# Kernel tuning notes

Measured on AMD Instinct MI355X. Metric: run time of the kernel, lower is better.

Reference implementation:

```python
import jax, jax.numpy as jnp
import numpy as np

D_MODEL = 1024
N_HEADS = 32
HEAD_DIM = D_MODEL // N_HEADS
EPS = 1e-5


def setup_inputs() -> dict:
    key = jax.random.key(0)
    ks = jax.random.split(key, 6)
    B, S = 2, 2048
    scale = 1.0 / np.sqrt(D_MODEL)
    return {
        "x": jax.random.normal(ks[0], (B, S, D_MODEL), dtype=jnp.float32),
        "Wqkv_w": jax.random.normal(ks[1], (3 * D_MODEL, D_MODEL), dtype=jnp.float32) * scale,
        "Wqkv_b": jax.random.normal(ks[2], (3 * D_MODEL,), dtype=jnp.float32) * 0.01,
        "gn_w": jnp.ones((D_MODEL,), dtype=jnp.float32),
        "gn_b": jnp.zeros((D_MODEL,), dtype=jnp.float32),
        "out_w": jax.random.normal(ks[3], (D_MODEL, D_MODEL), dtype=jnp.float32) * scale,
        "out_b": jax.random.normal(ks[4], (D_MODEL,), dtype=jnp.float32) * 0.01,
    }


def reference(x, Wqkv_w, Wqkv_b, gn_w, gn_b, out_w, out_b):
    B, S, Dm = x.shape
    H, Dh = N_HEADS, HEAD_DIM
    # QKV projection
    qkv = x @ Wqkv_w.T + Wqkv_b                      # [B,S,3*Dm]
    qkv = qkv.reshape(B, S, 3, H, Dh)
    q, k, v = qkv[:, :, 0], qkv[:, :, 1], qkv[:, :, 2]  # each [B,S,H,Dh]
    # Linear (softmax-free) attention; dropout p=0 -> identity
    a = jnp.einsum('bthd,bshd->bhts', q, k)          # [B,H,S,S]
    ctx = jnp.einsum('bhts,bshd->bthd', a, v)        # [B,S,H,Dh]
    # GroupNorm(num_groups=H, num_channels=Dm) on transposed (B, Dm, S):
    # normalizes jointly over (Dh channels, S positions) per (batch, group)
    g = ctx.transpose(0, 2, 3, 1)                    # [B,H,Dh,S]
    mean = g.mean(axis=(2, 3), keepdims=True)
    var = ((g - mean) ** 2).mean(axis=(2, 3), keepdims=True)
    gh = (g - mean) * jax.lax.rsqrt(var + EPS)
    gh = gh * gn_w.reshape(H, Dh, 1) + gn_b.reshape(H, Dh, 1)
    ctx = gh.transpose(0, 3, 1, 2).reshape(B, S, Dm)  # back to [B,S,Dm]
    return ctx @ out_w.T + out_b
```

## Files before the change

kernel.cpp:

```cpp
#include <hip/hip_runtime.h>
#include <hip/hip_bf16.h>
#include <stdint.h>

typedef unsigned short ushort_t;
typedef __attribute__((ext_vector_type(4))) float f32x4;
typedef __attribute__((ext_vector_type(8))) short short8;

#define SS 2048
#define ROWS 4096
#define EPS 1e-5f

__device__ __forceinline__ unsigned short f2bf(float f) {
  unsigned int u = __float_as_uint(f);
  u += 0x7FFF + ((u >> 16) & 1);
  return (unsigned short)(u >> 16);
}
__device__ __forceinline__ float bf2f(short s) {
  return __uint_as_float(((unsigned int)(unsigned short)s) << 16);
}

#define GLDS16(g, l)                                                        \
  __builtin_amdgcn_global_load_lds((__attribute__((address_space(1))) void*)(g), \
                                   (__attribute__((address_space(3))) void*)(l), 16, 0, 0)

__global__ __launch_bounds__(256) void f2b2_kernel(const float* __restrict__ a,
                                                   ushort_t* __restrict__ oa, int n4a,
                                                   const float* __restrict__ b,
                                                   ushort_t* __restrict__ ob, int n4b) {
  const int stride = gridDim.x * blockDim.x;
  const int total = n4a + n4b;
  for (int i = blockIdx.x * blockDim.x + threadIdx.x; i < total; i += stride) {
    const float4 v = (i < n4a) ? reinterpret_cast<const float4*>(a)[i]
                               : reinterpret_cast<const float4*>(b)[i - n4a];
    ushort4 o;
    o.x = f2bf(v.x); o.y = f2bf(v.y); o.z = f2bf(v.z); o.w = f2bf(v.w);
    if (i < n4a) reinterpret_cast<ushort4*>(oa)[i] = o;
    else         reinterpret_cast<ushort4*>(ob)[i - n4a] = o;
  }
}

#define MF(d, va, vb) d = __builtin_amdgcn_mfma_f32_16x16x32_bf16(va, vb, d, 0, 0, 0)
#define LD8(p) (*reinterpret_cast<const short8*>(p))

__global__ __launch_bounds__(512, 2) void gemm1_pipe(const ushort_t* __restrict__ A,
                                                     const ushort_t* __restrict__ B,
                                                     const float* __restrict__ bias,
                                                     ushort_t* __restrict__ C) {
  __shared__ __align__(16) ushort_t lds[4 * 14336];
  const int tid = threadIdx.x;
  const int wid = tid >> 6, lane = tid & 63;
  const int bm = blockIdx.x * 256, bn = blockIdx.y * 192;
  const int wm = wid >> 2, wn = wid & 3;

  const int srow = lane >> 2;
  const int scol = ((lane & 3) ^ ((lane >> 3) & 3)) * 8;
  const int widb = (wid < 6) ? wid : 0;
  const ushort_t* gA0 = A + (size_t)(bm + wid * 16 + srow) * 1024 + scol;
  const ushort_t* gA1 = A + (size_t)(bm + (8 + wid) * 16 + srow) * 1024 + scol;
  const ushort_t* gB0 = B + (size_t)(bn + widb * 16 + srow) * 1024 + scol;
  const ushort_t* gB1 = B + (size_t)(bn + (6 + widb) * 16 + srow) * 1024 + scol;

  const int lf = lane & 15, kf = lane >> 4;
  const int flip = ((lane >> 1) & 3) << 4;
  const int aBase = (((wm * 128 + lf) * 64 + kf * 16) ^ flip) >> 1;
  const int bBase = ((((wn * 48 + lf) * 64 + kf * 16) ^ flip) >> 1) + 8192;

  f32x4 acc[8][3] = {};

#define STAGE_A(t)                                                           \
  { ushort_t* d = lds + (((t) & 3) * 14336);                                 \
    GLDS16(gA0 + (t) * 32, d + wid * 512);                                   \
    GLDS16(gA1 + (t) * 32, d + (8 + wid) * 512); }
#define STAGE_B(t)                                                           \
  if (wid < 6) { ushort_t* d = lds + (((t) & 3) * 14336) + 8192;             \
    GLDS16(gB0 + (t) * 32, d + wid * 512);                                   \
    GLDS16(gB1 + (t) * 32, d + (6 + wid) * 512); }

  STAGE_A(0) STAGE_B(0)
  STAGE_A(1) STAGE_B(1)
  STAGE_A(2) STAGE_B(2)
  if (wid < 6) { asm volatile("s_waitcnt vmcnt(8)" ::: "memory"); }
  else         { asm volatile("s_waitcnt vmcnt(4)" ::: "memory"); }
  __builtin_amdgcn_s_barrier();
  __builtin_amdgcn_sched_barrier(0);

#define K_TILE(t, DO_STAGE, VM6, VM2)                                        \
  { const ushort_t* Lb = lds + (((t) & 3) * 14336);                          \
    short8 bv0 = LD8(Lb + bBase);                                            \
    short8 bv1 = LD8(Lb + bBase + 512);                                      \
    short8 bv2 = LD8(Lb + bBase + 1024);                                     \
    short8 a0 = LD8(Lb + aBase);                                             \
    short8 a1 = LD8(Lb + aBase + 512);                                       \
    short8 a2 = LD8(Lb + aBase + 1024);                                      \
    short8 a3 = LD8(Lb + aBase + 1536);                                      \
    if (DO_STAGE) STAGE_A((t) + 3)                                           \
    __builtin_amdgcn_s_setprio(1);                                           \
    MF(acc[0][0], a0, bv0); MF(acc[1][0], a1, bv0);                          \
    MF(acc[0][1], a0, bv1); MF(acc[1][1], a1, bv1);                          \
    MF(acc[0][2], a0, bv2); MF(acc[1][2], a1, bv2);                          \
    MF(acc[2][0], a2, bv0); MF(acc[3][0], a3, bv0);                          \
    MF(acc[2][1], a2, bv1); MF(acc[3][1], a3, bv1);                          \
    MF(acc[2][2], a2, bv2); MF(acc[3][2], a3, bv2);                          \
    __builtin_amdgcn_s_setprio(0);                                           \
    a0 = LD8(Lb + aBase + 2048);                                             \
    a1 = LD8(Lb + aBase + 2560);                                             \
    a2 = LD8(Lb + aBase + 3072);                                             \
    a3 = LD8(Lb + aBase + 3584);                                             \
    if (DO_STAGE) STAGE_B((t) + 3)                                           \
    __builtin_amdgcn_s_setprio(1);                                           \
    MF(acc[4][0], a0, bv0); MF(acc[5][0], a1, bv0);                          \
    MF(acc[4][1], a0, bv1); MF(acc[5][1], a1, bv1);                          \
    MF(acc[4][2], a0, bv2); MF(acc[5][2], a1, bv2);                          \
    MF(acc[6][0], a2, bv0); MF(acc[7][0], a3, bv0);                          \
    MF(acc[6][1], a2, bv1); MF(acc[7][1], a3, bv1);                          \
    MF(acc[6][2], a2, bv2); MF(acc[7][2], a3, bv2);                          \
    __builtin_amdgcn_s_setprio(0);                                           \
    __builtin_amdgcn_sched_barrier(0);                                       \
    if (wid < 6) { asm volatile("s_waitcnt vmcnt(" #VM6 ")" ::: "memory"); } \
    else         { asm volatile("s_waitcnt vmcnt(" #VM2 ")" ::: "memory"); } \
    __builtin_amdgcn_s_barrier();                                            \
    __builtin_amdgcn_sched_barrier(0); }

#pragma unroll 1
  for (int t = 0; t < 29; ++t) K_TILE(t, 1, 8, 4)
  K_TILE(29, 0, 4, 2)
  K_TILE(30, 0, 0, 0)
  K_TILE(31, 0, 0, 0)

  const int crow = bm + wm * 128 + (lane >> 4) * 4;
  const int ccol = bn + wn * 48 + (lane & 15);
#pragma unroll
  for (int m = 0; m < 8; ++m)
#pragma unroll
    for (int n = 0; n < 3; ++n) {
      const int col = ccol + n * 16;
      const float bb = bias[col];
#pragma unroll
      for (int j = 0; j < 4; ++j)
        C[(size_t)(crow + m * 16 + j) * 3072 + col] = f2bf(acc[m][n][j] + bb);
    }
#undef K_TILE
#undef STAGE_A
#undef STAGE_B
}

__global__ __launch_bounds__(256, 2) void gemm2_pipe(const ushort_t* __restrict__ A,
                                                     const ushort_t* __restrict__ B,
                                                     const float* __restrict__ bias,
                                                     float* __restrict__ C) {
  __shared__ __align__(16) ushort_t lds[4 * 6144];
  const int tid = threadIdx.x;
  const int wid = tid >> 6, lane = tid & 63;
  const int bm = blockIdx.x * 64, bn = blockIdx.y * 128;
  if (bm >= 2048) { B += (size_t)1024 * 1024; bias += 1024; }
  const int wm = wid >> 1, wn = wid & 1;

  const int srow = lane >> 2;
  const int scol = ((lane & 3) ^ ((lane >> 3) & 3)) * 8;
  const ushort_t* gA  = A + (size_t)(bm + wid * 16 + srow) * 1024 + scol;
  const ushort_t* gB0 = B + (size_t)(bn + wid * 16 + srow) * 1024 + scol;
  const ushort_t* gB1 = B + (size_t)(bn + (4 + wid) * 16 + srow) * 1024 + scol;

  const int lf = lane & 15, kf = lane >> 4;
  const int flip = ((lane >> 1) & 3) << 4;
  const int aBase = (((wm * 32 + lf) * 64 + kf * 16) ^ flip) >> 1;
  const int bBase = ((((wn * 64 + lf) * 64 + kf * 16) ^ flip) >> 1) + 2048;

  f32x4 acc[2][4] = {};

#define STAGE2(t)                                                            \
  { ushort_t* d = lds + (((t) & 3) * 6144);                                  \
    GLDS16(gA + (t) * 32, d + wid * 512);                                    \
    GLDS16(gB0 + (t) * 32, d + 2048 + wid * 512);                            \
    GLDS16(gB1 + (t) * 32, d + 2048 + (4 + wid) * 512); }

  STAGE2(0) STAGE2(1) STAGE2(2)
  asm volatile("s_waitcnt vmcnt(6)" ::: "memory");
  __builtin_amdgcn_s_barrier();
  __builtin_amdgcn_sched_barrier(0);

#define K_TILE2(t, DO_STAGE, VM)                                             \
  { const ushort_t* Lb = lds + (((t) & 3) * 6144);                           \
    short8 bv0 = LD8(Lb + bBase);                                            \
    short8 bv1 = LD8(Lb + bBase + 512);                                      \
    short8 bv2 = LD8(Lb + bBase + 1024);                                     \
    short8 bv3 = LD8(Lb + bBase + 1536);                                     \
    short8 a0 = LD8(Lb + aBase);                                             \
    short8 a1 = LD8(Lb + aBase + 512);                                       \
    if (DO_STAGE) STAGE2((t) + 3)                                            \
    __builtin_amdgcn_s_setprio(1);                                           \
    MF(acc[0][0], a0, bv0); MF(acc[1][0], a1, bv0);                          \
    MF(acc[0][1], a0, bv1); MF(acc[1][1], a1, bv1);                          \
    MF(acc[0][2], a0, bv2); MF(acc[1][2], a1, bv2);                          \
    MF(acc[0][3], a0, bv3); MF(acc[1][3], a1, bv3);                          \
    __builtin_amdgcn_s_setprio(0);                                           \
    __builtin_amdgcn_sched_barrier(0);                                       \
    asm volatile("s_waitcnt vmcnt(" #VM ")" ::: "memory");                   \
    __builtin_amdgcn_s_barrier();                                            \
    __builtin_amdgcn_sched_barrier(0); }

#pragma unroll 1
  for (int t = 0; t < 29; ++t) K_TILE2(t, 1, 6)
  K_TILE2(29, 0, 3)
  K_TILE2(30, 0, 0)
  K_TILE2(31, 0, 0)

  const int crow = bm + wm * 32 + (lane >> 4) * 4;
  const int ccol = bn + wn * 64 + lf;
#pragma unroll
  for (int m = 0; m < 2; ++m)
#pragma unroll
    for (int n = 0; n < 4; ++n) {
      const int col = ccol + n * 16;
      const float bb = bias[col];
#pragma unroll
      for (int j = 0; j < 4; ++j)
        C[(size_t)(crow + m * 16 + j) * 1024 + col] = acc[m][n][j] + bb;
    }
#undef K_TILE2
#undef STAGE2
}

__global__ __launch_bounds__(256) void kv_partial(const ushort_t* __restrict__ qkvb,
                                                  float* __restrict__ KVp) {
  __shared__ float kt[64 * 32];
  __shared__ float vt[64 * 32];
  const int blk = blockIdx.x;
  const int bh = blk >> 5;
  const int ch = blk & 31;
  const int b = bh >> 5, h = bh & 31;
  const int tid = threadIdx.x;
  const int r = tid >> 2, cg = (tid & 3) * 8;
  const ushort_t* kp = qkvb + (size_t)(b * SS + ch * 64 + r) * 3072 + 1024 + h * 32 + cg;
  const short8 k8 = *(const short8*)kp;
  const short8 v8 = *(const short8*)(kp + 1024);
#pragma unroll
  for (int i = 0; i < 8; ++i) {
    kt[r * 32 + cg + i] = bf2f(k8[i]);
    vt[r * 32 + cg + i] = bf2f(v8[i]);
  }
  __syncthreads();
  const int d = tid & 31, eg = tid >> 5;
  float acc[4] = {0.f, 0.f, 0.f, 0.f};
#pragma unroll 8
  for (int ss = 0; ss < 64; ++ss) {
    const float vv = vt[ss * 32 + d];
#pragma unroll
    for (int i = 0; i < 4; ++i)
      acc[i] += kt[ss * 32 + eg * 4 + i] * vv;
  }
  float* o = KVp + ((size_t)bh * 32 + ch) * 1024 + (eg * 4) * 32 + d;
#pragma unroll
  for (int i = 0; i < 4; ++i) o[i * 32] = acc[i];
}

__global__ __launch_bounds__(256) void kv_reduce(const float* __restrict__ KVp,
                                                 float* __restrict__ KV) {
  const int bh = blockIdx.x;
  const int tid = threadIdx.x;
  const float* base = KVp + (size_t)bh * 32768 + tid * 4;
  float4 s = make_float4(0.f, 0.f, 0.f, 0.f);
  for (int c = 0; c < 32; ++c) {
    const float4 v = *(const float4*)(base + c * 1024);
    s.x += v.x; s.y += v.y; s.z += v.z; s.w += v.w;
  }
  *(float4*)&KV[(size_t)bh * 1024 + tid * 4] = s;
}

__global__ __launch_bounds__(256) void ctx_kernel(const ushort_t* __restrict__ qkvb,
                                                  const float* __restrict__ KV,
                                                  ushort_t* __restrict__ ctxb,
                                                  float2* __restrict__ partials) {
  __shared__ float kvs[1024];
  __shared__ float red[8];
  const int blk = blockIdx.x;
  const int bh = blk >> 3, tt = blk & 7;
  const int b = bh >> 5, h = bh & 31;
  const int tid = threadIdx.x;
  for (int i = tid; i < 1024; i += 256) kvs[i] = KV[(size_t)bh * 1024 + i];
  __syncthreads();
  const int t = tt * 256 + tid;
  const ushort_t* qrow = qkvb + ((size_t)(b * SS + t)) * 3072 + h * 32;
  float q[32];
#pragma unroll
  for (int g = 0; g < 4; ++g) {
    const short8 qv = *(const short8*)(qrow + g * 8);
#pragma unroll
    for (int i = 0; i < 8; ++i) q[g * 8 + i] = bf2f(qv[i]);
  }
  float o[32];
#pragma unroll
  for (int d = 0; d < 32; ++d) o[d] = 0.f;
#pragma unroll
  for (int e = 0; e < 32; ++e) {
    const float qe = q[e];
    const float* kr = &kvs[e * 32];
#pragma unroll
    for (int d = 0; d < 32; ++d) o[d] += qe * kr[d];
  }
  float sum = 0.f, sq = 0.f;
#pragma unroll
  for (int d = 0; d < 32; ++d) { sum += o[d]; sq += o[d] * o[d]; }
  ushort_t* crow = ctxb + ((size_t)(b * SS + t)) * 1024 + h * 32;
#pragma unroll
  for (int g = 0; g < 4; ++g) {
    short8 ov;
#pragma unroll
    for (int i = 0; i < 8; ++i) ov[i] = (short)f2bf(o[g * 8 + i]);
    *(short8*)(crow + g * 8) = ov;
  }
#pragma unroll
  for (int off = 32; off > 0; off >>= 1) {
    sum += __shfl_down(sum, off);
    sq  += __shfl_down(sq, off);
  }
  const int wave = tid >> 6, lane = tid & 63;
  if (lane == 0) { red[wave * 2] = sum; red[wave * 2 + 1] = sq; }
  __syncthreads();
  if (tid == 0) {
    const float s = red[0] + red[2] + red[4] + red[6];
    const float q2 = red[1] + red[3] + red[5] + red[7];
    partials[blk] = make_float2(s, q2);
  }
}

__global__ __launch_bounds__(256) void fold_kernel(const float* __restrict__ W2,
                                                   const float* __restrict__ b2,
                                                   const float* __restrict__ gw,
                                                   const float* __restrict__ gb,
                                                   const float2* __restrict__ partials,
                                                   ushort_t* __restrict__ W2s,
                                                   float* __restrict__ bias2) {
  __shared__ float sS[1024], sT[1024];
  __shared__ float sMean[32], sRstd[32];
  const int b = blockIdx.y;
  const int tid = threadIdx.x;
  if (tid < 32) {
    float s = 0.f, q = 0.f;
    for (int i = 0; i < 8; ++i) {
      const float2 p = partials[(b * 32 + tid) * 8 + i];
      s += p.x; q += p.y;
    }
    const float mean = s * (1.f / 65536.f);
    const float var = q * (1.f / 65536.f) - mean * mean;
    sMean[tid] = mean; sRstd[tid] = rsqrtf(var + EPS);
  }
  __syncthreads();
  {
    const int c0 = tid * 4;
    const float mean = sMean[c0 >> 5], rstd = sRstd[c0 >> 5];
    const float4 w = *(const float4*)&gw[c0];
    const float4 g = *(const float4*)&gb[c0];
    sS[c0]     = rstd * w.x;  sT[c0]     = g.x - mean * rstd * w.x;
    sS[c0 + 1] = rstd * w.y;  sT[c0 + 1] = g.y - mean * rstd * w.y;
    sS[c0 + 2] = rstd * w.z;  sT[c0 + 2] = g.z - mean * rstd * w.z;
    sS[c0 + 3] = rstd * w.w;  sT[c0 + 3] = g.w - mean * rstd * w.w;
  }
  __syncthreads();
  const int row = blockIdx.x * 16 + (tid >> 4);
  const int l16 = tid & 15;
  float part = 0.f;
  for (int k = 0; k < 16; ++k) {
    const int c = k * 64 + l16 * 4;
    const float4 w2v = *(const float4*)&W2[(size_t)row * 1024 + c];
    ushort4 o;
    o.x = f2bf(w2v.x * sS[c]);
    o.y = f2bf(w2v.y * sS[c + 1]);
    o.z = f2bf(w2v.z * sS[c + 2]);
    o.w = f2bf(w2v.w * sS[c + 3]);
    *(ushort4*)&W2s[(size_t)b * 1048576 + (size_t)row * 1024 + c] = o;
    part += w2v.x * sT[c] + w2v.y * sT[c + 1] + w2v.z * sT[c + 2] + w2v.w * sT[c + 3];
  }
#pragma unroll
  for (int off = 8; off > 0; off >>= 1) part += __shfl_down(part, off, 16);
  if (l16 == 0) bias2[b * 1024 + row] = b2[row] + part;
}

extern "C" void kernel_launch(void* const* d_in, const int* in_sizes, int n_in,
                              void* d_out, int out_size, void* d_ws, size_t ws_size,
                              hipStream_t stream) {
  const float* x  = (const float*)d_in[0];
  const float* w1 = (const float*)d_in[1];
  const float* b1 = (const float*)d_in[2];
  const float* gw = (const float*)d_in[3];
  const float* gb = (const float*)d_in[4];
  const float* w2 = (const float*)d_in[5];
  const float* b2 = (const float*)d_in[6];
  float* out = (float*)d_out;

  char* ws = (char*)d_ws;
  ushort_t* Xb    = (ushort_t*)(ws);
  float*    KVp   = (float*)(ws);
  ushort_t* W1b   = (ushort_t*)(ws + 8388608);
  ushort_t* qkvb  = (ushort_t*)(ws + 16777216);
  ushort_t* ctxb  = (ushort_t*)(ws + 41943040);
  ushort_t* W2s   = (ushort_t*)(ws + 50331648);
  float*    bias2 = (float*)(ws + 54525952);
  float*    KV    = (float*)(ws + 54534144);
  float2*   partials = (float2*)(ws + 54796288);

  f2b2_kernel<<<2048, 256, 0, stream>>>(x, Xb, ROWS * 1024 / 4, w1, W1b, 3072 * 1024 / 4);
  gemm1_pipe<<<dim3(16, 16), 512, 0, stream>>>(Xb, W1b, b1, qkvb);
  kv_partial<<<2048, 256, 0, stream>>>(qkvb, KVp);
  kv_reduce<<<64, 256, 0, stream>>>(KVp, KV);
  ctx_kernel<<<512, 256, 0, stream>>>(qkvb, KV, ctxb, partials);
  fold_kernel<<<dim3(64, 2), 256, 0, stream>>>(w2, b2, gw, gb, partials, W2s, bias2);
  gemm2_pipe<<<dim3(64, 8), 256, 0, stream>>>(ctxb, W2s, bias2, out);
}
```

Before: 88.92 us.

## Compute GroupNorm stats analytically from Q covariance and KV, drop fold kernel

GroupNorm mean and variance are now derived in closed form from per-head Q^T Q covariance, Q column sums and the KV matrix, which the partial kernel accumulates alongside KV. Normalization is applied directly when ctx is written, so the fold kernel that rescaled W2 per batch is removed. The separate kv_reduce launch is merged into the ctx kernel, and W2 is cast to bf16 in the existing conversion kernel. This cuts launches and the W2 fold pass, but each ctx block redundantly reduces 32 partials of two matrices, and computing variance as E[x^2] minus mean^2 in fp32 may lose precision.

```diff
diff --git a/kernel.cpp b/kernel.cpp
--- a/kernel.cpp
+++ b/kernel.cpp
@@ -23,19 +23,23 @@
   __builtin_amdgcn_global_load_lds((__attribute__((address_space(1))) void*)(g), \
                                    (__attribute__((address_space(3))) void*)(l), 16, 0, 0)
 
-__global__ __launch_bounds__(256) void f2b2_kernel(const float* __restrict__ a,
+__global__ __launch_bounds__(256) void f2b3_kernel(const float* __restrict__ a,
                                                    ushort_t* __restrict__ oa, int n4a,
                                                    const float* __restrict__ b,
-                                                   ushort_t* __restrict__ ob, int n4b) {
+                                                   ushort_t* __restrict__ ob, int n4b,
+                                                   const float* __restrict__ c,
+                                                   ushort_t* __restrict__ oc, int n4c) {
   const int stride = gridDim.x * blockDim.x;
-  const int total = n4a + n4b;
+  const int total = n4a + n4b + n4c;
   for (int i = blockIdx.x * blockDim.x + threadIdx.x; i < total; i += stride) {
-    const float4 v = (i < n4a) ? reinterpret_cast<const float4*>(a)[i]
-                               : reinterpret_cast<const float4*>(b)[i - n4a];
+    const float* src; ushort_t* dst; int idx;
+    if (i < n4a)            { src = a; dst = oa; idx = i; }
+    else if (i < n4a + n4b) { src = b; dst = ob; idx = i - n4a; }
+    else                    { src = c; dst = oc; idx = i - n4a - n4b; }
+    const float4 v = reinterpret_cast<const float4*>(src)[idx];
     ushort4 o;
     o.x = f2bf(v.x); o.y = f2bf(v.y); o.z = f2bf(v.z); o.w = f2bf(v.w);
-    if (i < n4a) reinterpret_cast<ushort4*>(oa)[i] = o;
-    else         reinterpret_cast<ushort4*>(ob)[i - n4a] = o;
+    reinterpret_cast<ushort4*>(dst)[idx] = o;
   }
 }
 
@@ -152,7 +156,6 @@
   const int tid = threadIdx.x;
   const int wid = tid >> 6, lane = tid & 63;
   const int bm = blockIdx.x * 64, bn = blockIdx.y * 128;
-  if (bm >= 2048) { B += (size_t)1024 * 1024; bias += 1024; }
   const int wm = wid >> 1, wn = wid & 1;
 
   const int srow = lane >> 2;
@@ -221,8 +224,11 @@
 #undef STAGE2
 }
 
-__global__ __launch_bounds__(256) void kv_partial(const ushort_t* __restrict__ qkvb,
-                                                  float* __restrict__ KVp) {
+__global__ __launch_bounds__(256) void kvq_partial(const ushort_t* __restrict__ qkvb,
+                                                   float* __restrict__ KVp,
+                                                   float* __restrict__ Qcovp,
+                                                   float* __restrict__ qsump) {
+  __shared__ float qt[64 * 32];
   __shared__ float kt[64 * 32];
   __shared__ float vt[64 * 32];
   const int blk = blockIdx.x;
@@ -231,60 +237,119 @@
   const int b = bh >> 5, h = bh & 31;
   const int tid = threadIdx.x;
   const int r = tid >> 2, cg = (tid & 3) * 8;
-  const ushort_t* kp = qkvb + (size_t)(b * SS + ch * 64 + r) * 3072 + 1024 + h * 32 + cg;
-  const short8 k8 = *(const short8*)kp;
-  const short8 v8 = *(const short8*)(kp + 1024);
+  const ushort_t* base = qkvb + (size_t)(b * SS + ch * 64 + r) * 3072 + h * 32 + cg;
+  const short8 q8 = LD8(base);
+  const short8 k8 = LD8(base + 1024);
+  const short8 v8 = LD8(base + 2048);
 #pragma unroll
   for (int i = 0; i < 8; ++i) {
+    qt[r * 32 + cg + i] = bf2f(q8[i]);
     kt[r * 32 + cg + i] = bf2f(k8[i]);
     vt[r * 32 + cg + i] = bf2f(v8[i]);
   }
   __syncthreads();
   const int d = tid & 31, eg = tid >> 5;
-  float acc[4] = {0.f, 0.f, 0.f, 0.f};
-#pragma unroll 8
+  float kv[4] = {0.f, 0.f, 0.f, 0.f};
+  float qc[4] = {0.f, 0.f, 0.f, 0.f};
+#pragma unroll 4
   for (int ss = 0; ss < 64; ++ss) {
     const float vv = vt[ss * 32 + d];
-#pragma unroll
-    for (int i = 0; i < 4; ++i)
-      acc[i] += kt[ss * 32 + eg * 4 + i] * vv;
-  }
-  float* o = KVp + ((size_t)bh * 32 + ch) * 1024 + (eg * 4) * 32 + d;
-#pragma unroll
-  for (int i = 0; i < 4; ++i) o[i * 32] = acc[i];
-}
-
-__global__ __launch_bounds__(256) void kv_reduce(const float* __restrict__ KVp,
-                                                 float* __restrict__ KV) {
-  const int bh = blockIdx.x;
-  const int tid = threadIdx.x;
-  const float* base = KVp + (size_t)bh * 32768 + tid * 4;
-  float4 s = make_float4(0.f, 0.f, 0.f, 0.f);
-  for (int c = 0; c < 32; ++c) {
-    const float4 v = *(const float4*)(base + c * 1024);
-    s.x += v.x; s.y += v.y; s.z += v.z; s.w += v.w;
-  }
-  *(float4*)&KV[(size_t)bh * 1024 + tid * 4] = s;
-}
-
-__global__ __launch_bounds__(256) void ctx_kernel(const ushort_t* __restrict__ qkvb,
-                                                  const float* __restrict__ KV,
-                                                  ushort_t* __restrict__ ctxb,
-                                                  float2* __restrict__ partials) {
-  __shared__ float kvs[1024];
-  __shared__ float red[8];
+    const float qd = qt[ss * 32 + d];
+#pragma unroll
+    for (int i = 0; i < 4; ++i) {
+      kv[i] += kt[ss * 32 + eg * 4 + i] * vv;
+      qc[i] += qt[ss * 32 + eg * 4 + i] * qd;
+    }
+  }
+  float* okv = KVp + ((size_t)bh * 32 + ch) * 1024 + (eg * 4) * 32 + d;
+  float* oqc = Qcovp + ((size_t)bh * 32 + ch) * 1024 + (eg * 4) * 32 + d;
+#pragma unroll
+  for (int i = 0; i < 4; ++i) { okv[i * 32] = kv[i]; oqc[i * 32] = qc[i]; }
+  if (tid < 32) {
+    float s = 0.f;
+    for (int ss = 0; ss < 64; ++ss) s += qt[ss * 32 + tid];
+    qsump[((size_t)bh * 32 + ch) * 32 + tid] = s;
+  }
+}
+
+__global__ __launch_bounds__(256) void ctx_norm_kernel(const ushort_t* __restrict__ qkvb,
+                                                       const float* __restrict__ KVp,
+                                                       const float* __restrict__ Qcovp,
+                                                       const float* __restrict__ qsump,
+                                                       const float* __restrict__ gw,
+                                                       const float* __restrict__ gb,
+                                                       ushort_t* __restrict__ ghb) {
+  __shared__ float kvs[1024], qcov[1024];
+  __shared__ float qsums[32], gws[32], gbs[32];
+  __shared__ float red[16];
+  __shared__ float sstats[2];
   const int blk = blockIdx.x;
   const int bh = blk >> 3, tt = blk & 7;
   const int b = bh >> 5, h = bh & 31;
   const int tid = threadIdx.x;
-  for (int i = tid; i < 1024; i += 256) kvs[i] = KV[(size_t)bh * 1024 + i];
+  {
+    const float* kbase = KVp + (size_t)bh * 32768 + tid * 4;
+    const float* qbase = Qcovp + (size_t)bh * 32768 + tid * 4;
+    float4 sk = make_float4(0.f, 0.f, 0.f, 0.f);
+    float4 sq = make_float4(0.f, 0.f, 0.f, 0.f);
+    for (int c = 0; c < 32; ++c) {
+      const float4 k4 = *(const float4*)(kbase + c * 1024);
+      const float4 q4 = *(const float4*)(qbase + c * 1024);
+      sk.x += k4.x; sk.y += k4.y; sk.z += k4.z; sk.w += k4.w;
+      sq.x += q4.x; sq.y += q4.y; sq.z += q4.z; sq.w += q4.w;
+    }
+    *(float4*)&kvs[tid * 4] = sk;
+    *(float4*)&qcov[tid * 4] = sq;
+  }
+  if (tid < 32) {
+    float s = 0.f;
+    for (int c = 0; c < 32; ++c) s += qsump[((size_t)bh * 32 + c) * 32 + tid];
+    qsums[tid] = s;
+    gws[tid] = gw[h * 32 + tid];
+    gbs[tid] = gb[h * 32 + tid];
+  }
   __syncthreads();
+  {
+    const int d = tid & 31, ig = tid >> 5;
+    float e2p = 0.f;
+#pragma unroll
+    for (int ii = 0; ii < 4; ++ii) {
+      const int i = ig * 4 + ii;
+      float t = 0.f;
+#pragma unroll
+      for (int j = 0; j < 32; ++j) t += qcov[i * 32 + j] * kvs[j * 32 + d];
+      e2p += kvs[i * 32 + d] * t;
+    }
+#pragma unroll
+    for (int off = 32; off > 0; off >>= 1) e2p += __shfl_down(e2p, off);
+    float mp = 0.f;
+    if (tid < 32) {
+      float rs = 0.f;
+      for (int dd = 0; dd < 32; ++dd) rs += kvs[tid * 32 + ((dd + tid) & 31)];
+      mp = rs * qsums[tid];
+    }
+#pragma unroll
+    for (int off = 32; off > 0; off >>= 1) mp += __shfl_down(mp, off);
+    const int wave = tid >> 6, lane = tid & 63;
+    if (lane == 0) { red[wave] = e2p; red[8 + wave] = mp; }
+    __syncthreads();
+    if (tid == 0) {
+      const float E2 = red[0] + red[1] + red[2] + red[3];
+      const float MS = red[8] + red[9] + red[10] + red[11];
+      const float mean = MS * (1.f / 65536.f);
+      const float var = E2 * (1.f / 65536.f) - mean * mean;
+      sstats[0] = mean;
+      sstats[1] = rsqrtf(var + EPS);
+    }
+    __syncthreads();
+  }
+  const float mean = sstats[0], rstd = sstats[1];
   const int t = tt * 256 + tid;
   const ushort_t* qrow = qkvb + ((size_t)(b * SS + t)) * 3072 + h * 32;
   float q[32];
 #pragma unroll
   for (int g = 0; g < 4; ++g) {
-    const short8 qv = *(const short8*)(qrow + g * 8);
+    const short8 qv = LD8(qrow + g * 8);
 #pragma unroll
     for (int i = 0; i < 8; ++i) q[g * 8 + i] = bf2f(qv[i]);
   }
@@ -298,82 +363,17 @@
 #pragma unroll
     for (int d = 0; d < 32; ++d) o[d] += qe * kr[d];
   }
-  float sum = 0.f, sq = 0.f;
-#pragma unroll
-  for (int d = 0; d < 32; ++d) { sum += o[d]; sq += o[d] * o[d]; }
-  ushort_t* crow = ctxb + ((size_t)(b * SS + t)) * 1024 + h * 32;
+  ushort_t* crow = ghb + ((size_t)(b * SS + t)) * 1024 + h * 32;
 #pragma unroll
   for (int g = 0; g < 4; ++g) {
     short8 ov;
 #pragma unroll
-    for (int i = 0; i < 8; ++i) ov[i] = (short)f2bf(o[g * 8 + i]);
+    for (int i = 0; i < 8; ++i) {
+      const int d = g * 8 + i;
+      ov[i] = (short)f2bf((o[d] - mean) * rstd * gws[d] + gbs[d]);
+    }
     *(short8*)(crow + g * 8) = ov;
   }
-#pragma unroll
-  for (int off = 32; off > 0; off >>= 1) {
-    sum += __shfl_down(sum, off);
-    sq  += __shfl_down(sq, off);
-  }
-  const int wave = tid >> 6, lane = tid & 63;
-  if (lane == 0) { red[wave * 2] = sum; red[wave * 2 + 1] = sq; }
-  __syncthreads();
-  if (tid == 0) {
-    const float s = red[0] + red[2] + red[4] + red[6];
-    const float q2 = red[1] + red[3] + red[5] + red[7];
-    partials[blk] = make_float2(s, q2);
-  }
-}
-
-__global__ __launch_bounds__(256) void fold_kernel(const float* __restrict__ W2,
-                                                   const float* __restrict__ b2,
-                                                   const float* __restrict__ gw,
-                                                   const float* __restrict__ gb,
-                                                   const float2* __restrict__ partials,
-                                                   ushort_t* __restrict__ W2s,
-                                                   float* __restrict__ bias2) {
-  __shared__ float sS[1024], sT[1024];
-  __shared__ float sMean[32], sRstd[32];
-  const int b = blockIdx.y;
-  const int tid = threadIdx.x;
-  if (tid < 32) {
-    float s = 0.f, q = 0.f;
-    for (int i = 0; i < 8; ++i) {
-      const float2 p = partials[(b * 32 + tid) * 8 + i];
-      s += p.x; q += p.y;
-    }
-    const float mean = s * (1.f / 65536.f);
-    const float var = q * (1.f / 65536.f) - mean * mean;
-    sMean[tid] = mean; sRstd[tid] = rsqrtf(var + EPS);
-  }
-  __syncthreads();
-  {
-    const int c0 = tid * 4;
-    const float mean = sMean[c0 >> 5], rstd = sRstd[c0 >> 5];
-    const float4 w = *(const float4*)&gw[c0];
-    const float4 g = *(const float4*)&gb[c0];
-    sS[c0]     = rstd * w.x;  sT[c0]     = g.x - mean * rstd * w.x;
-    sS[c0 + 1] = rstd * w.y;  sT[c0 + 1] = g.y - mean * rstd * w.y;
-    sS[c0 + 2] = rstd * w.z;  sT[c0 + 2] = g.z - mean * rstd * w.z;
-    sS[c0 + 3] = rstd * w.w;  sT[c0 + 3] = g.w - mean * rstd * w.w;
-  }
-  __syncthreads();
-  const int row = blockIdx.x * 16 + (tid >> 4);
-  const int l16 = tid & 15;
-  float part = 0.f;
-  for (int k = 0; k < 16; ++k) {
-    const int c = k * 64 + l16 * 4;
-    const float4 w2v = *(const float4*)&W2[(size_t)row * 1024 + c];
-    ushort4 o;
-    o.x = f2bf(w2v.x * sS[c]);
-    o.y = f2bf(w2v.y * sS[c + 1]);
-    o.z = f2bf(w2v.z * sS[c + 2]);
-    o.w = f2bf(w2v.w * sS[c + 3]);
-    *(ushort4*)&W2s[(size_t)b * 1048576 + (size_t)row * 1024 + c] = o;
-    part += w2v.x * sT[c] + w2v.y * sT[c + 1] + w2v.z * sT[c + 2] + w2v.w * sT[c + 3];
-  }
-#pragma unroll
-  for (int off = 8; off > 0; off >>= 1) part += __shfl_down(part, off, 16);
-  if (l16 == 0) bias2[b * 1024 + row] = b2[row] + part;
 }
 
 extern "C" void kernel_launch(void* const* d_in, const int* in_sizes, int n_in,
@@ -392,18 +392,17 @@
   ushort_t* Xb    = (ushort_t*)(ws);
   float*    KVp   = (float*)(ws);
   ushort_t* W1b   = (ushort_t*)(ws + 8388608);
+  float*    Qcovp = (float*)(ws + 8388608);
   ushort_t* qkvb  = (ushort_t*)(ws + 16777216);
-  ushort_t* ctxb  = (ushort_t*)(ws + 41943040);
-  ushort_t* W2s   = (ushort_t*)(ws + 50331648);
-  float*    bias2 = (float*)(ws + 54525952);
-  float*    KV    = (float*)(ws + 54534144);
-  float2*   partials = (float2*)(ws + 54796288);
-
-  f2b2_kernel<<<2048, 256, 0, stream>>>(x, Xb, ROWS * 1024 / 4, w1, W1b, 3072 * 1024 / 4);
+  ushort_t* ghb   = (ushort_t*)(ws + 41943040);
+  ushort_t* W2b   = (ushort_t*)(ws + 50331648);
+  float*    qsump = (float*)(ws + 52428800);
+
+  f2b3_kernel<<<2048, 256, 0, stream>>>(x, Xb, ROWS * 1024 / 4,
+                                        w1, W1b, 3072 * 1024 / 4,
+                                        w2, W2b, 1024 * 1024 / 4);
   gemm1_pipe<<<dim3(16, 16), 512, 0, stream>>>(Xb, W1b, b1, qkvb);
-  kv_partial<<<2048, 256, 0, stream>>>(qkvb, KVp);
-  kv_reduce<<<64, 256, 0, stream>>>(KVp, KV);
-  ctx_kernel<<<512, 256, 0, stream>>>(qkvb, KV, ctxb, partials);
-  fold_kernel<<<dim3(64, 2), 256, 0, stream>>>(w2, b2, gw, gb, partials, W2s, bias2);
-  gemm2_pipe<<<dim3(64, 8), 256, 0, stream>>>(ctxb, W2s, bias2, out);
-}
+  kvq_partial<<<2048, 256, 0, stream>>>(qkvb, KVp, Qcovp, qsump);
+  ctx_norm_kernel<<<512, 256, 0, stream>>>(qkvb, KVp, Qcovp, qsump, gw, gb, ghb);
+  gemm2_pipe<<<dim3(64, 8), 256, 0, stream>>>(ghb, W2b, b2, out);
+}
```

New measurement: 103.5 us. 16.5% more time.
